# Performance work log

Hardware: AMD Instinct MI355X
Metric: run time of the kernel (lower is better)

Reference implementation:

```python
import jax, jax.numpy as jnp
import numpy as np

S = 4      # num_residual_streams
V = 1      # num_input_views
ITERS = 20 # sinkhorn iters
B = 2      # batch
N = 4096   # seq len
D = 2048   # dim (num_fracs=1 so dim_eff == dim)


def setup_inputs() -> dict:
    key = jax.random.key(0)
    ks = jax.random.split(key, 6)
    return dict(
        residuals=jax.random.normal(ks[0], (B * S, N, D), jnp.float32),
        gamma=0.1 * jax.random.normal(ks[1], (S * D,), jnp.float32),
        dyn_alpha_fn=0.02 * jax.random.normal(ks[2], (S * D, S * (S + V)), jnp.float32),
        static_alpha=jax.random.normal(ks[3], (S, S + V), jnp.float32),
        pre_branch_scale=0.01 * jnp.ones((1,), jnp.float32),
        residual_scale=0.01 * jnp.ones((1,), jnp.float32),
        dyn_beta_fn=0.02 * jax.random.normal(ks[4], (S * D, S), jnp.float32),
        static_beta=jax.random.normal(ks[5], (S,), jnp.float32),
        h_post_scale=jnp.float32(0.01),
    )


def _sinkhorn(log_a, iters):
    # alternating row/col normalization in log space over last two axes
    def body(_, la):
        la = la - jax.scipy.special.logsumexp(la, axis=-2, keepdims=True)
        return la - jax.scipy.special.logsumexp(la, axis=-1, keepdims=True)
    return jnp.exp(jax.lax.fori_loop(0, iters, body, log_a))


def reference(residuals, gamma, dyn_alpha_fn, static_alpha, pre_branch_scale,
              residual_scale, dyn_beta_fn, static_beta, h_post_scale):
    bs, n, d = residuals.shape
    b = bs // S
    # '(b s) n d -> b n s d'
    r = residuals.reshape(b, S, n, d).transpose(0, 2, 1, 3)  # [b,n,S,d]
    flat = r.reshape(b, n, S * d)
    # RMSNorm: F.normalize(x, dim=-1) * sqrt(S*d) * (gamma + 1)
    nrm = flat / jnp.maximum(jnp.linalg.norm(flat, axis=-1, keepdims=True), 1e-12)
    normed = nrm * jnp.sqrt(jnp.float32(S * d)) * (gamma + 1.0)  # [b,n,S*d]

    wc = (normed @ dyn_alpha_fn).reshape(b, n, S, S + V)  # dynamic gate weights
    alpha_scale = jnp.concatenate([
        jnp.broadcast_to(pre_branch_scale, (V,)),
        jnp.broadcast_to(residual_scale, (S,)),
    ])  # [S+V]
    alpha = wc * alpha_scale + static_alpha  # [b,n,S,S+V]
    alpha_pre = jax.nn.sigmoid(alpha[..., :V])            # [b,n,S,V]
    alpha_res = _sinkhorn(alpha[..., V:], ITERS)          # doubly-stochastic [b,n,S,S]
    alpha_full = jnp.concatenate([alpha_pre, alpha_res], axis=-1)  # [b,n,S,1+S]

    # mix streams: '... s t, ... s d -> ... t d'
    mix = jnp.einsum('bnst,bnsd->bntd', alpha_full, r)  # [b,n,1+S,d]
    branch_input = mix[..., 0, :]       # [b,n,d]
    res_mix = mix[..., 1:, :]           # [b,n,S,d]

    beta = jax.nn.sigmoid((normed @ dyn_beta_fn) * h_post_scale + static_beta) * 2.0  # [b,n,S]

    # branch = identity -> branch_output == branch_input
    # depth connection: 'b n d, b n s -> b n s d', then add residual streams
    out = branch_input[..., None, :] * beta[..., :, None] + res_mix  # [b,n,S,d]
    # 'b n s d -> (b s) n d'
    return out.transpose(0, 2, 1, 3).reshape(b * S, n, d)
```

## Files before the change

kernel.cpp:

```cpp
#include <hip/hip_runtime.h>
#include <hip/hip_bf16.h>

typedef float f32x4 __attribute__((ext_vector_type(4)));
typedef float f32x16 __attribute__((ext_vector_type(16)));
typedef unsigned int u32;
typedef u32 u32x2 __attribute__((ext_vector_type(2)));
typedef u32 u32x4 __attribute__((ext_vector_type(4)));
typedef short bf16x8 __attribute__((ext_vector_type(8)));

#define SD 8192
#define NROWS 8192
#define NN 4096
#define DD 2048
#define DTP 4104

__device__ __forceinline__ u32 bfr(float f) {
    u32 u = __float_as_uint(f);
    return (u + 0x7fffu + ((u >> 16) & 1u)) >> 16;
}
__device__ __forceinline__ float blo(u32 u) { return __uint_as_float(u << 16); }
__device__ __forceinline__ float bhi(u32 u) { return __uint_as_float(u & 0xffff0000u); }

__global__ void k0_prep(const float* __restrict__ gamma,
                        const float* __restrict__ daf,
                        const float* __restrict__ dbf,
                        unsigned short* __restrict__ Wfrag) {
    int idx = blockIdx.x * 256 + threadIdx.x;
    if (idx >= 32 * SD) return;
    const int e    = idx & 7;
    const int lane = (idx >> 3) & 63;
    const int stg  = idx >> 9;
    const int outk = lane & 31;
    const int j    = stg * 16 + ((lane >> 5) & 1) * 8 + e;
    unsigned short v = 0;
    if (outk < 24) {
        float g = gamma[j] + 1.0f;
        float w = (outk < 20) ? daf[j * 20 + outk] : dbf[j * 4 + (outk - 20)];
        v = (unsigned short)bfr(w * g);
    }
    Wfrag[idx] = v;
}

__global__ __launch_bounds__(512) void kf(const float* __restrict__ res,
                                          const unsigned short* __restrict__ Wfrag,
                                          const float* __restrict__ sa,
                                          const float* __restrict__ sb,
                                          const float* __restrict__ pbs,
                                          const float* __restrict__ rsc,
                                          const float* __restrict__ hps,
                                          float* __restrict__ out) {
    __shared__ u32 dTp[4][DTP];
    __shared__ float pc[8][4][32];
    __shared__ float red[4][32];
    __shared__ float ssqw[8];
    __shared__ float coefS[4][16];

    const int tid  = threadIdx.x;
    const int wv   = tid >> 6;
    const int lane = tid & 63;
    const int row0 = blockIdx.x * 4;
    const int b    = row0 >> 12;
    const int n0   = row0 & (NN - 1);
    const int r    = tid >> 7;
    const int rem  = tid & 127;

    {
        const float* rowbase = res + ((size_t)(b * 4) * NN + (n0 + r)) * DD;
        const u32* abase = &dTp[lane & 3][wv * 64 + (lane >> 5) * 4];
        const unsigned short* wb0 = Wfrag + (size_t)lane * 8;

        f32x16 acc;
#pragma unroll
        for (int i = 0; i < 16; ++i) acc[i] = 0.f;
        float ssq = 0.f;

        f32x4 vA0, vA1, vB0, vB1;

#define LDV(V0, V1, T)                                                        \
        do {                                                                  \
            const int j0_ = (T) * 1024 + rem * 8;                             \
            const int s_ = j0_ >> 11, d_ = j0_ & 2047;                        \
            const float* p_ = rowbase + (size_t)s_ * NN * DD + d_;            \
            V0 = *(const f32x4*)(p_);                                         \
            V1 = *(const f32x4*)(p_ + 4);                                     \
        } while (0)

#define CONSUME(V0, V1, T)                                                    \
        do {                                                                  \
            ssq += V0.x * V0.x + V0.y * V0.y + V0.z * V0.z + V0.w * V0.w;     \
            ssq += V1.x * V1.x + V1.y * V1.y + V1.z * V1.z + V1.w * V1.w;     \
            u32 c0_, c1_, c2_, c3_;                                           \
            asm("v_cvt_pk_bf16_f32 %0, %1, %2" : "=v"(c0_) : "v"(V0.x), "v"(V0.y)); \
            asm("v_cvt_pk_bf16_f32 %0, %1, %2" : "=v"(c1_) : "v"(V0.z), "v"(V0.w)); \
            asm("v_cvt_pk_bf16_f32 %0, %1, %2" : "=v"(c2_) : "v"(V1.x), "v"(V1.y)); \
            asm("v_cvt_pk_bf16_f32 %0, %1, %2" : "=v"(c3_) : "v"(V1.z), "v"(V1.w)); \
            *(u32x4*)&dTp[r][(T) * 512 + rem * 4] = (u32x4){c0_, c1_, c2_, c3_}; \
        } while (0)

#define BLOAD(BU, T)                                                          \
        do {                                                                  \
            _Pragma("unroll")                                                 \
            for (int s8_ = 0; s8_ < 8; ++s8_)                                 \
                BU[s8_] = *(const u32x4*)(wb0 + (size_t)(((T) * 64 + wv * 8 + s8_) * 64) * 8); \
        } while (0)

#define MMT(BU, T)                                                            \
        do {                                                                  \
            asm volatile("s_waitcnt lgkmcnt(0)" ::: "memory");                \
            __builtin_amdgcn_sched_barrier(0);                                \
            __builtin_amdgcn_s_barrier();                                     \
            _Pragma("unroll")                                                 \
            for (int s8_ = 0; s8_ < 8; ++s8_) {                               \
                const u32x4 au_ = *(const u32x4*)(abase + (T) * 512 + s8_ * 8); \
                acc = __builtin_amdgcn_mfma_f32_32x32x16_bf16(                \
                    __builtin_bit_cast(bf16x8, au_),                          \
                    __builtin_bit_cast(bf16x8, BU[s8_]), acc, 0, 0, 0);       \
            }                                                                 \
            __builtin_amdgcn_sched_barrier(0);                                \
        } while (0)

        LDV(vA0, vA1, 0);
        LDV(vB0, vB1, 1);
#pragma unroll 1
        for (int tp = 0; tp < 4; ++tp) {
            const int t0 = tp * 2, t1 = t0 + 1;
            CONSUME(vA0, vA1, t0);
            u32x4 bu0[8];
            BLOAD(bu0, t0);
            if (t0 < 6) LDV(vA0, vA1, t0 + 2);
            MMT(bu0, t0);
            CONSUME(vB0, vB1, t1);
            u32x4 bu1[8];
            BLOAD(bu1, t1);
            if (t1 < 7) LDV(vB0, vB1, t1 + 2);
            MMT(bu1, t1);
        }
#undef LDV
#undef CONSUME
#undef BLOAD
#undef MMT

        ssq += __shfl_xor(ssq, 1);  ssq += __shfl_xor(ssq, 2);
        ssq += __shfl_xor(ssq, 4);  ssq += __shfl_xor(ssq, 8);
        ssq += __shfl_xor(ssq, 16); ssq += __shfl_xor(ssq, 32);
        if (lane == 0) ssqw[wv] = ssq;
        if (lane < 32) {
#pragma unroll
            for (int gg = 0; gg < 4; ++gg) pc[wv][gg][lane] = acc[gg];
        }
    }
    __syncthreads();
    if (tid < 128) {
        const int rr = tid >> 5, c = tid & 31;
        float s = 0.f;
#pragma unroll
        for (int w = 0; w < 8; ++w) s += pc[w][rr][c];
        red[rr][c] = s;
    }
    __syncthreads();

    if (wv == 0) {
        const int rr = lane >> 4, l = lane & 15, s = l >> 2, t = l & 3;
        const float ssqr  = ssqw[2 * rr] + ssqw[2 * rr + 1];
        const float scale = 90.50966799187809f / fmaxf(sqrtf(ssqr), 1e-12f);
        const float P  = red[rr][s * 5 + t + 1];
        const float P0 = red[rr][s * 5];
        const float Pb = red[rr][20 + t];
        float la = scale * P * rsc[0] + sa[s * 5 + t + 1];
        const float a0 = scale * P0 * pbs[0] + sa[s * 5];
        const float ap = 1.f / (1.f + __expf(-a0));
        const float bt = 2.f / (1.f + __expf(-(scale * Pb * hps[0] + sb[t])));
#pragma unroll
        for (int it = 0; it < 20; ++it) {
            float m = fmaxf(la, __shfl_xor(la, 4));
            m = fmaxf(m, __shfl_xor(m, 8));
            float e = __expf(la - m);
            e += __shfl_xor(e, 4);
            e += __shfl_xor(e, 8);
            la -= m + __logf(e);
            m = fmaxf(la, __shfl_xor(la, 1));
            m = fmaxf(m, __shfl_xor(m, 2));
            e = __expf(la - m);
            e += __shfl_xor(e, 1);
            e += __shfl_xor(e, 2);
            la -= m + __logf(e);
        }
        coefS[rr][t * 4 + s] = ap * bt + __expf(la);
    }
    __syncthreads();

    float cf[16];
#pragma unroll
    for (int i = 0; i < 16; ++i) cf[i] = coefS[r][i];
    float* ob = out + ((size_t)(b * 4) * NN + (n0 + r)) * DD;
#pragma unroll 1
    for (int qq = 0; qq < 4; ++qq) {
        const int dp = (rem + 128 * qq) * 2;
        f32x4 dv4[4];
#pragma unroll
        for (int s = 0; s < 4; ++s) {
            u32x2 u = *(const u32x2*)&dTp[r][s * 1024 + dp];
            dv4[s] = (f32x4){blo(u[0]), bhi(u[0]), blo(u[1]), bhi(u[1])};
        }
#pragma unroll
        for (int t = 0; t < 4; ++t) {
            f32x4 o = cf[t * 4 + 0] * dv4[0];
            o += cf[t * 4 + 1] * dv4[1];
            o += cf[t * 4 + 2] * dv4[2];
            o += cf[t * 4 + 3] * dv4[3];
            __builtin_nontemporal_store(o, (f32x4*)(ob + (size_t)t * NN * DD + dp * 2));
        }
    }
}

extern "C" void kernel_launch(void* const* d_in, const int* in_sizes, int n_in,
                              void* d_out, int out_size, void* d_ws, size_t ws_size,
                              hipStream_t stream) {
    const float* residuals = (const float*)d_in[0];
    const float* gamma     = (const float*)d_in[1];
    const float* daf       = (const float*)d_in[2];
    const float* sa        = (const float*)d_in[3];
    const float* pbs       = (const float*)d_in[4];
    const float* rsc       = (const float*)d_in[5];
    const float* dbf       = (const float*)d_in[6];
    const float* sb        = (const float*)d_in[7];
    const float* hps       = (const float*)d_in[8];
    float* out = (float*)d_out;

    unsigned short* Wfrag = (unsigned short*)d_ws;

    k0_prep<<<1024, 256, 0, stream>>>(gamma, daf, dbf, Wfrag);
    kf<<<NROWS / 4, 512, 0, stream>>>(residuals, Wfrag, sa, sb, pbs, rsc, hps, out);
}
```

Before: 122.1 us.

## Process one full stream per stage, halving barriers in the GEMV pipeline

The fused norm+projection loop now loads 2048 elements per thread-group stage (four f32x4 per thread, one whole stream plane) instead of 1024, cutting the stage count from 8 to 4. Each stage's MFMA work is split into two groups of eight, and the next global loads are issued between them. Block barriers drop from eight to four. In exchange, more vector registers hold in-flight loads, which may lower occupancy, and the LDS write and read index layout changes.

```diff
diff --git a/kernel.cpp b/kernel.cpp
--- a/kernel.cpp
+++ b/kernel.cpp
@@ -12,6 +12,7 @@
 #define NROWS 8192
 #define NN 4096
 #define DD 2048
+#define PLANE ((size_t)NN * DD)
 #define DTP 4104
 
 __device__ __forceinline__ u32 bfr(float f) {
@@ -66,7 +67,7 @@
 
     {
         const float* rowbase = res + ((size_t)(b * 4) * NN + (n0 + r)) * DD;
-        const u32* abase = &dTp[lane & 3][wv * 64 + (lane >> 5) * 4];
+        const u32* abase = &dTp[lane & 3][wv * 128 + (lane >> 5) * 4];
         const unsigned short* wb0 = Wfrag + (size_t)lane * 8;
 
         f32x16 acc;
@@ -74,71 +75,102 @@
         for (int i = 0; i < 16; ++i) acc[i] = 0.f;
         float ssq = 0.f;
 
-        f32x4 vA0, vA1, vB0, vB1;
-
-#define LDV(V0, V1, T)                                                        \
-        do {                                                                  \
-            const int j0_ = (T) * 1024 + rem * 8;                             \
-            const int s_ = j0_ >> 11, d_ = j0_ & 2047;                        \
-            const float* p_ = rowbase + (size_t)s_ * NN * DD + d_;            \
+        f32x4 vA0, vA1, vA2, vA3, vB0, vB1, vB2, vB3;
+
+#define LDV(V0, V1, V2, V3, T)                                                \
+        do {                                                                  \
+            const float* p_ = rowbase + (size_t)(T) * PLANE + rem * 8;        \
             V0 = *(const f32x4*)(p_);                                         \
             V1 = *(const f32x4*)(p_ + 4);                                     \
-        } while (0)
-
-#define CONSUME(V0, V1, T)                                                    \
+            V2 = *(const f32x4*)(p_ + 1024);                                  \
+            V3 = *(const f32x4*)(p_ + 1028);                                  \
+        } while (0)
+
+#define CONSUME(V0, V1, V2, V3, T)                                            \
         do {                                                                  \
             ssq += V0.x * V0.x + V0.y * V0.y + V0.z * V0.z + V0.w * V0.w;     \
             ssq += V1.x * V1.x + V1.y * V1.y + V1.z * V1.z + V1.w * V1.w;     \
+            ssq += V2.x * V2.x + V2.y * V2.y + V2.z * V2.z + V2.w * V2.w;     \
+            ssq += V3.x * V3.x + V3.y * V3.y + V3.z * V3.z + V3.w * V3.w;     \
             u32 c0_, c1_, c2_, c3_;                                           \
             asm("v_cvt_pk_bf16_f32 %0, %1, %2" : "=v"(c0_) : "v"(V0.x), "v"(V0.y)); \
             asm("v_cvt_pk_bf16_f32 %0, %1, %2" : "=v"(c1_) : "v"(V0.z), "v"(V0.w)); \
             asm("v_cvt_pk_bf16_f32 %0, %1, %2" : "=v"(c2_) : "v"(V1.x), "v"(V1.y)); \
             asm("v_cvt_pk_bf16_f32 %0, %1, %2" : "=v"(c3_) : "v"(V1.z), "v"(V1.w)); \
-            *(u32x4*)&dTp[r][(T) * 512 + rem * 4] = (u32x4){c0_, c1_, c2_, c3_}; \
-        } while (0)
-
-#define BLOAD(BU, T)                                                          \
+            *(u32x4*)&dTp[r][(T) * 1024 + rem * 4] = (u32x4){c0_, c1_, c2_, c3_}; \
+            asm("v_cvt_pk_bf16_f32 %0, %1, %2" : "=v"(c0_) : "v"(V2.x), "v"(V2.y)); \
+            asm("v_cvt_pk_bf16_f32 %0, %1, %2" : "=v"(c1_) : "v"(V2.z), "v"(V2.w)); \
+            asm("v_cvt_pk_bf16_f32 %0, %1, %2" : "=v"(c2_) : "v"(V3.x), "v"(V3.y)); \
+            asm("v_cvt_pk_bf16_f32 %0, %1, %2" : "=v"(c3_) : "v"(V3.z), "v"(V3.w)); \
+            *(u32x4*)&dTp[r][(T) * 1024 + 512 + rem * 4] = (u32x4){c0_, c1_, c2_, c3_}; \
+        } while (0)
+
+#define BLOAD(BU, T, G)                                                       \
         do {                                                                  \
             _Pragma("unroll")                                                 \
             for (int s8_ = 0; s8_ < 8; ++s8_)                                 \
-                BU[s8_] = *(const u32x4*)(wb0 + (size_t)(((T) * 64 + wv * 8 + s8_) * 64) * 8); \
-        } while (0)
-
-#define MMT(BU, T)                                                            \
-        do {                                                                  \
-            asm volatile("s_waitcnt lgkmcnt(0)" ::: "memory");                \
-            __builtin_amdgcn_sched_barrier(0);                                \
-            __builtin_amdgcn_s_barrier();                                     \
+                BU[s8_] = *(const u32x4*)(wb0 + (size_t)(((T) * 128 + wv * 16 + (G) * 8 + s8_) * 64) * 8); \
+        } while (0)
+
+#define MMG(BU, T, G)                                                         \
+        do {                                                                  \
             _Pragma("unroll")                                                 \
             for (int s8_ = 0; s8_ < 8; ++s8_) {                               \
-                const u32x4 au_ = *(const u32x4*)(abase + (T) * 512 + s8_ * 8); \
+                const u32x4 au_ = *(const u32x4*)(abase + (T) * 1024 + ((G) * 8 + s8_) * 8); \
                 acc = __builtin_amdgcn_mfma_f32_32x32x16_bf16(                \
                     __builtin_bit_cast(bf16x8, au_),                          \
                     __builtin_bit_cast(bf16x8, BU[s8_]), acc, 0, 0, 0);       \
             }                                                                 \
+        } while (0)
+
+#define BARRIER_LGKM                                                          \
+        do {                                                                  \
+            asm volatile("s_waitcnt lgkmcnt(0)" ::: "memory");                \
             __builtin_amdgcn_sched_barrier(0);                                \
-        } while (0)
-
-        LDV(vA0, vA1, 0);
-        LDV(vB0, vB1, 1);
+            __builtin_amdgcn_s_barrier();                                     \
+        } while (0)
+
+        LDV(vA0, vA1, vA2, vA3, 0);
+        LDV(vB0, vB1, vB2, vB3, 1);
 #pragma unroll 1
-        for (int tp = 0; tp < 4; ++tp) {
+        for (int tp = 0; tp < 2; ++tp) {
             const int t0 = tp * 2, t1 = t0 + 1;
-            CONSUME(vA0, vA1, t0);
-            u32x4 bu0[8];
-            BLOAD(bu0, t0);
-            if (t0 < 6) LDV(vA0, vA1, t0 + 2);
-            MMT(bu0, t0);
-            CONSUME(vB0, vB1, t1);
-            u32x4 bu1[8];
-            BLOAD(bu1, t1);
-            if (t1 < 7) LDV(vB0, vB1, t1 + 2);
-            MMT(bu1, t1);
+            CONSUME(vA0, vA1, vA2, vA3, t0);
+            {
+                u32x4 bu0[8];
+                BLOAD(bu0, t0, 0);
+                BARRIER_LGKM;
+                MMG(bu0, t0, 0);
+            }
+            __builtin_amdgcn_sched_barrier(0);
+            {
+                u32x4 bu1[8];
+                BLOAD(bu1, t0, 1);
+                if (tp == 0) LDV(vA0, vA1, vA2, vA3, 2);
+                MMG(bu1, t0, 1);
+            }
+            __builtin_amdgcn_sched_barrier(0);
+            CONSUME(vB0, vB1, vB2, vB3, t1);
+            {
+                u32x4 bu0[8];
+                BLOAD(bu0, t1, 0);
+                BARRIER_LGKM;
+                MMG(bu0, t1, 0);
+            }
+            __builtin_amdgcn_sched_barrier(0);
+            {
+                u32x4 bu1[8];
+                BLOAD(bu1, t1, 1);
+                if (tp == 0) LDV(vB0, vB1, vB2, vB3, 3);
+                MMG(bu1, t1, 1);
+            }
+            __builtin_amdgcn_sched_barrier(0);
         }
 #undef LDV
 #undef CONSUME
 #undef BLOAD
-#undef MMT
+#undef MMG
+#undef BARRIER_LGKM
 
         ssq += __shfl_xor(ssq, 1);  ssq += __shfl_xor(ssq, 2);
         ssq += __shfl_xor(ssq, 4);  ssq += __shfl_xor(ssq, 8);
```

New measurement: 172.0 us. 40.8% more time.

## Deepen global load prefetch to three stages and fold cross-wave reduction into wave 0

Applied to the files above, without the earlier changes.

The main loop now keeps three register-buffered tiles of residual loads in flight instead of two, issuing each load three tiles ahead so global memory latency is better hidden behind the MFMA work. The loop is restructured into two triple iterations plus a peeled tail. Separately, the partial-sum reduction across waves is moved into wave 0's gate computation, which removes a shared-memory stage and one block barrier. The extra in-flight registers raise VGPR pressure, which may reduce occupancy.

```diff
diff --git a/kernel.cpp b/kernel.cpp
--- a/kernel.cpp
+++ b/kernel.cpp
@@ -51,7 +51,6 @@
                                           float* __restrict__ out) {
     __shared__ u32 dTp[4][DTP];
     __shared__ float pc[8][4][32];
-    __shared__ float red[4][32];
     __shared__ float ssqw[8];
     __shared__ float coefS[4][16];
 
@@ -74,7 +73,7 @@
         for (int i = 0; i < 16; ++i) acc[i] = 0.f;
         float ssq = 0.f;
 
-        f32x4 vA0, vA1, vB0, vB1;
+        f32x4 vA0, vA1, vB0, vB1, vC0, vC1;
 
 #define LDV(V0, V1, T)                                                        \
         do {                                                                  \
@@ -121,19 +120,43 @@
 
         LDV(vA0, vA1, 0);
         LDV(vB0, vB1, 1);
+        LDV(vC0, vC1, 2);
 #pragma unroll 1
-        for (int tp = 0; tp < 4; ++tp) {
-            const int t0 = tp * 2, t1 = t0 + 1;
+        for (int tp = 0; tp < 2; ++tp) {
+            const int t0 = tp * 3, t1 = t0 + 1, t2 = t0 + 2;
             CONSUME(vA0, vA1, t0);
-            u32x4 bu0[8];
-            BLOAD(bu0, t0);
-            if (t0 < 6) LDV(vA0, vA1, t0 + 2);
-            MMT(bu0, t0);
+            {
+                u32x4 bu[8];
+                BLOAD(bu, t0);
+                LDV(vA0, vA1, t0 + 3);
+                MMT(bu, t0);
+            }
             CONSUME(vB0, vB1, t1);
-            u32x4 bu1[8];
-            BLOAD(bu1, t1);
-            if (t1 < 7) LDV(vB0, vB1, t1 + 2);
-            MMT(bu1, t1);
+            {
+                u32x4 bu[8];
+                BLOAD(bu, t1);
+                LDV(vB0, vB1, t1 + 3);
+                MMT(bu, t1);
+            }
+            CONSUME(vC0, vC1, t2);
+            {
+                u32x4 bu[8];
+                BLOAD(bu, t2);
+                if (tp == 0) LDV(vC0, vC1, 5);
+                MMT(bu, t2);
+            }
+        }
+        CONSUME(vA0, vA1, 6);
+        {
+            u32x4 bu[8];
+            BLOAD(bu, 6);
+            MMT(bu, 6);
+        }
+        CONSUME(vB0, vB1, 7);
+        {
+            u32x4 bu[8];
+            BLOAD(bu, 7);
+            MMT(bu, 7);
         }
 #undef LDV
 #undef CONSUME
@@ -150,22 +173,18 @@
         }
     }
     __syncthreads();
-    if (tid < 128) {
-        const int rr = tid >> 5, c = tid & 31;
-        float s = 0.f;
-#pragma unroll
-        for (int w = 0; w < 8; ++w) s += pc[w][rr][c];
-        red[rr][c] = s;
-    }
-    __syncthreads();
 
     if (wv == 0) {
         const int rr = lane >> 4, l = lane & 15, s = l >> 2, t = l & 3;
         const float ssqr  = ssqw[2 * rr] + ssqw[2 * rr + 1];
         const float scale = 90.50966799187809f / fmaxf(sqrtf(ssqr), 1e-12f);
-        const float P  = red[rr][s * 5 + t + 1];
-        const float P0 = red[rr][s * 5];
-        const float Pb = red[rr][20 + t];
+        float P = 0.f, P0 = 0.f, Pb = 0.f;
+#pragma unroll
+        for (int w = 0; w < 8; ++w) {
+            P  += pc[w][rr][s * 5 + t + 1];
+            P0 += pc[w][rr][s * 5];
+            Pb += pc[w][rr][20 + t];
+        }
         float la = scale * P * rsc[0] + sa[s * 5 + t + 1];
         const float a0 = scale * P0 * pbs[0] + sa[s * 5];
         const float ap = 1.f / (1.f + __expf(-a0));
```

After: 167.7 us. +37.4%, slower.
